# Optimization experiments

Hardware: AMD Instinct MI355X
Metric: run time of the kernel (lower is better)

The kernel has to match this reference:

```python
import jax, jax.numpy as jnp
import numpy as np

B, S, D_MODEL, N_HEADS, D_FEAT = 8, 1024, 1024, 16, 64


def setup_inputs() -> dict:
    key = jax.random.key(0)
    ks = jax.random.split(key, 5)
    sin = jax.random.normal(ks[0], (B, S, D_MODEL), dtype=jnp.float32)
    mask = jnp.ones((B, S), dtype=bool)  # only its presence matters in the original
    # Per-head Linear(d_model -> d_feature): weight stored as [H, d_model, d_feature]
    lim = 1.0 / np.sqrt(D_MODEL)
    Wx = jax.random.uniform(ks[1], (N_HEADS, D_MODEL, D_FEAT), dtype=jnp.float32, minval=-lim, maxval=lim)
    bx = jax.random.uniform(ks[2], (N_HEADS, D_FEAT), dtype=jnp.float32, minval=-lim, maxval=lim)
    # Output projection Linear(H*d_feature -> d_model), stored as [in, out]
    lim_p = 1.0 / np.sqrt(N_HEADS * D_FEAT)
    Wp = jax.random.uniform(ks[3], (N_HEADS * D_FEAT, D_MODEL), dtype=jnp.float32, minval=-lim_p, maxval=lim_p)
    bp = jax.random.uniform(ks[4], (D_MODEL,), dtype=jnp.float32, minval=-lim_p, maxval=lim_p)
    return {"sin": sin, "mask": mask, "Wx": Wx, "bx": bx, "Wp": Wp, "bp": bp}


def reference(sin, mask, Wx, bx, Wp, bp):
    # All heads batched: per-head linear projection  [B,H,S,F]
    x = jnp.einsum("bsd,hdf->bhsf", sin, Wx) + bx[None, :, None, :]
    # Cosine-similarity scores: x x^T / (||x|| ||x||^T)  -> [B,H,S,S]
    norm = jnp.sqrt(jnp.sum(x * x, axis=-1, keepdims=True))  # [B,H,S,1]
    scores = jnp.einsum("bhsf,bhtf->bhst", x, x) / (norm * jnp.swapaxes(norm, -2, -1))
    # Original quirk: when mask is not None, entries that are exactly 0.0 get -inf
    scores = jnp.where(scores == 0.0, -jnp.inf, scores)
    p_attn = jax.nn.softmax(scores, axis=-1)
    out = jnp.einsum("bhst,bhtf->bhsf", p_attn, x)
    # Concat heads: [B,S,H*F]
    out = jnp.transpose(out, (0, 2, 1, 3)).reshape(out.shape[0], out.shape[2], -1)
    return out @ Wp + bp
```

## Files before the change

### kernel.cpp

```cpp
#include <hip/hip_runtime.h>
#include <hip/hip_bf16.h>
#include <math.h>

typedef _Float16 f16;
typedef _Float16 half8 __attribute__((ext_vector_type(8)));
typedef float f32x4 __attribute__((ext_vector_type(4)));
typedef float f32x16 __attribute__((ext_vector_type(16)));
typedef unsigned int u32;

#define NB 8
#define NS 1024
#define DM 1024
#define NH 16
#define NF 64

__global__ __launch_bounds__(256) void csin_kernel(const float* __restrict__ in, f16* __restrict__ out) {
  long gid = (long)blockIdx.x * 256 + threadIdx.x;
  const float4* p = (const float4*)(in + gid * 8);
  float4 a = p[0], b = p[1];
  half8 v;
  v[0] = (f16)a.x; v[1] = (f16)a.y; v[2] = (f16)a.z; v[3] = (f16)a.w;
  v[4] = (f16)b.x; v[5] = (f16)b.y; v[6] = (f16)b.z; v[7] = (f16)b.w;
  *(half8*)(out + gid * 8) = v;
}

__global__ __launch_bounds__(256) void cwx_kernel(const float* __restrict__ Wx, f16* __restrict__ W2T) {
  __shared__ float T[64][65];
  int h = blockIdx.x >> 4, d0 = (blockIdx.x & 15) * 64;
  int tid = threadIdx.x;
  const float* src = Wx + ((size_t)h * 1024 + d0) * 64;
  int row = tid >> 2, cg = (tid & 3) * 16;
#pragma unroll
  for (int k = 0; k < 4; ++k) {
    float4 v = *(const float4*)(src + (size_t)row * 64 + cg + k * 4);
    T[row][cg + k * 4 + 0] = v.x;
    T[row][cg + k * 4 + 1] = v.y;
    T[row][cg + k * 4 + 2] = v.z;
    T[row][cg + k * 4 + 3] = v.w;
  }
  __syncthreads();
  int f = tid >> 2, dg = (tid & 3) * 16;
  f16 o[16];
#pragma unroll
  for (int j = 0; j < 16; ++j) o[j] = (f16)T[dg + j][f];
  *(half8*)(W2T + (size_t)(h * 64 + f) * DM + d0 + dg) = *(half8*)&o[0];
  *(half8*)(W2T + (size_t)(h * 64 + f) * DM + d0 + dg + 8) = *(half8*)&o[8];
}

__global__ __launch_bounds__(256) void cwp_kernel(const float* __restrict__ Wp, f16* __restrict__ WpT) {
  __shared__ float T[64][65];
  int n0 = (blockIdx.x >> 4) * 64, d0 = (blockIdx.x & 15) * 64;
  int tid = threadIdx.x;
  int row = tid >> 2, cg = (tid & 3) * 16;
#pragma unroll
  for (int k = 0; k < 4; ++k) {
    float4 v = *(const float4*)(Wp + (size_t)(d0 + row) * DM + n0 + cg + k * 4);
    T[row][cg + k * 4 + 0] = v.x;
    T[row][cg + k * 4 + 1] = v.y;
    T[row][cg + k * 4 + 2] = v.z;
    T[row][cg + k * 4 + 3] = v.w;
  }
  __syncthreads();
  int f = tid >> 2, dg = (tid & 3) * 16;
  f16 o[16];
#pragma unroll
  for (int j = 0; j < 16; ++j) o[j] = (f16)T[dg + j][f];
  *(half8*)(WpT + (size_t)(n0 + f) * DM + d0 + dg) = *(half8*)&o[0];
  *(half8*)(WpT + (size_t)(n0 + f) * DM + d0 + dg + 8) = *(half8*)&o[8];
}

template <int MODE>
__global__ __launch_bounds__(256) void gemm_kernel(const f16* __restrict__ A, const f16* __restrict__ Bt,
                                                   const float* __restrict__ bias, void* __restrict__ Cv) {
  __shared__ f16 As[128][64];
  __shared__ f16 Bs[128][64];
  int tid = threadIdx.x;
  int l = tid & 63, wv = tid >> 6;
  int wm = wv >> 1, wn = wv & 1;
  int xcd = blockIdx.x & 7, m = blockIdx.x >> 3;
  int bm = ((m >> 3) << 3) | xcd;
  int bn = m & 7;
  int lr = l & 15, lh = l >> 4;

  f32x4 acc[4][4];
#pragma unroll
  for (int i = 0; i < 4; ++i)
#pragma unroll
    for (int j = 0; j < 4; ++j) acc[i][j] = (f32x4)0.f;

  const f16* gA = A + (size_t)(bm * 128 + wv * 32 + (l >> 3)) * DM + (l & 7) * 8;
  const f16* gB = Bt + (size_t)(bn * 128 + wv * 32 + (l >> 3)) * DM + (l & 7) * 8;
  f16* ldsA = &As[wv * 32][0];
  f16* ldsB = &Bs[wv * 32][0];

  for (int k0 = 0; k0 < DM; k0 += 64) {
    __syncthreads();
#pragma unroll
    for (int c = 0; c < 4; ++c) {
      __builtin_amdgcn_global_load_lds(
          (const __attribute__((address_space(1))) void*)(gA + k0 + (size_t)c * 8 * DM),
          (__attribute__((address_space(3))) void*)(ldsA + c * 512), 16, 0, 0);
      __builtin_amdgcn_global_load_lds(
          (const __attribute__((address_space(1))) void*)(gB + k0 + (size_t)c * 8 * DM),
          (__attribute__((address_space(3))) void*)(ldsB + c * 512), 16, 0, 0);
    }
    __syncthreads();
#pragma unroll
    for (int ks = 0; ks < 2; ++ks) {
      half8 af[4], bf[4];
#pragma unroll
      for (int mi = 0; mi < 4; ++mi) af[mi] = *(const half8*)&As[wm * 64 + mi * 16 + lr][ks * 32 + lh * 8];
#pragma unroll
      for (int ni = 0; ni < 4; ++ni) bf[ni] = *(const half8*)&Bs[wn * 64 + ni * 16 + lr][ks * 32 + lh * 8];
#pragma unroll
      for (int mi = 0; mi < 4; ++mi)
#pragma unroll
        for (int ni = 0; ni < 4; ++ni)
          acc[mi][ni] = __builtin_amdgcn_mfma_f32_16x16x32_f16(af[mi], bf[ni], acc[mi][ni], 0, 0, 0);
    }
  }

#pragma unroll
  for (int mi = 0; mi < 4; ++mi)
#pragma unroll
    for (int ni = 0; ni < 4; ++ni) {
      int gc = bn * 128 + wn * 64 + ni * 16 + lr;
      float bv = bias[gc];
#pragma unroll
      for (int r = 0; r < 4; ++r) {
        int gr = bm * 128 + wm * 64 + mi * 16 + lh * 4 + r;
        float v = acc[mi][ni][r] + bv;
        if (MODE == 0) {
          f16* x = (f16*)Cv;
          int b = gr >> 10, s = gr & 1023, h = gc >> 6, f = gc & 63;
          x[(size_t)((b * NH + h) * NS + s) * NF + f] = (f16)v;
        } else {
          ((float*)Cv)[(size_t)gr * DM + gc] = v;
        }
      }
    }
}

__global__ __launch_bounds__(256) void transnorm_kernel(f16* __restrict__ x, f16* __restrict__ xT) {
  __shared__ f16 T[64][64];
  __shared__ float sinv[64];
  int bh = blockIdx.x >> 4, s0 = (blockIdx.x & 15) * 64;
  int tid = threadIdx.x;
  f16* xb = x + (size_t)bh * (NS * NF);
  half8 vv[2];
#pragma unroll
  for (int it = 0; it < 2; ++it) {
    int idx = it * 256 + tid;
    int sr = idx >> 3, fcb = idx & 7;
    half8 v = *(const half8*)(xb + (size_t)(s0 + sr) * NF + fcb * 8);
    vv[it] = v;
    *(half8*)&T[sr][((fcb ^ ((sr >> 3) & 7)) * 8)] = v;
    float s = 0.f;
#pragma unroll
    for (int j = 0; j < 8; ++j) {
      float u = (float)v[j];
      s += u * u;
    }
    s += __shfl_xor(s, 1, 64);
    s += __shfl_xor(s, 2, 64);
    s += __shfl_xor(s, 4, 64);
    if ((tid & 7) == 0) sinv[sr] = rsqrtf(s);
  }
  __syncthreads();
#pragma unroll
  for (int it = 0; it < 2; ++it) {
    int idx = it * 256 + tid;
    int fr = idx >> 3, scb = idx & 7;
    half8 v;
#pragma unroll
    for (int j = 0; j < 8; ++j) v[j] = T[scb * 8 + j][(((fr >> 3) ^ scb) * 8) + (fr & 7)];
    *(half8*)(xT + ((size_t)bh * NF + fr) * NS + s0 + scb * 8) = v;
  }
#pragma unroll
  for (int it = 0; it < 2; ++it) {
    int idx = it * 256 + tid;
    int sr = idx >> 3, fcb = idx & 7;
    float inv = sinv[sr];
    half8 v = vv[it], o;
#pragma unroll
    for (int j = 0; j < 8; ++j) o[j] = (f16)((float)v[j] * inv);
    *(half8*)(xb + (size_t)(s0 + sr) * NF + fcb * 8) = o;
  }
}

__global__ __launch_bounds__(256, 4) void attn_kernel(const f16* __restrict__ xn, const f16* __restrict__ xT,
                                                      f16* __restrict__ ao) {
  __shared__ f16 KB[2][4096];
  __shared__ f16 VB[2][4096];

  int tid = threadIdx.x;
  int l = tid & 63, wv = tid >> 6;
  int lq = l & 31, hi = l >> 5;
  int kq = hi * 8;
  int xcd = blockIdx.x & 7, m = blockIdx.x >> 3;
  int bh = ((m >> 3) << 3) | xcd;
  int q0 = (m & 7) * 128;
  const f16* xnb = xn + (size_t)bh * (NS * NF);
  const f16* xTb = xT + (size_t)bh * (NF * NS);

  int srow = wv * 8 + (l >> 3);
  int scol = ((l & 7) ^ (l >> 3)) * 8;
  const f16* gK0 = xnb + (size_t)srow * NF + scol;
  const f16* gV0 = xTb + (size_t)srow * NS + scol;

  half8 bq[4];
#pragma unroll
  for (int ks = 0; ks < 4; ++ks)
    bq[ks] = *(const half8*)(xnb + (size_t)(q0 + wv * 32 + lq) * NF + ks * 16 + kq);

  f32x16 accO[2];
  accO[0] = (f32x16)0.f;
  accO[1] = (f32x16)0.f;
  float rs = 0.f;

#define STAGE(buf, t0_)                                                                               \
  do {                                                                                                \
    __builtin_amdgcn_global_load_lds(                                                                 \
        (const __attribute__((address_space(1))) void*)(gK0 + (size_t)(t0_) * NF),                    \
        (__attribute__((address_space(3))) void*)(&KB[buf][wv * 512]), 16, 0, 0);                     \
    __builtin_amdgcn_global_load_lds(                                                                 \
        (const __attribute__((address_space(1))) void*)(gK0 + (size_t)(t0_ + 32) * NF),               \
        (__attribute__((address_space(3))) void*)(&KB[buf][2048 + wv * 512]), 16, 0, 0);              \
    __builtin_amdgcn_global_load_lds(                                                                 \
        (const __attribute__((address_space(1))) void*)(gV0 + (t0_)),                                 \
        (__attribute__((address_space(3))) void*)(&VB[buf][wv * 512]), 16, 0, 0);                     \
    __builtin_amdgcn_global_load_lds(                                                                 \
        (const __attribute__((address_space(1))) void*)(gV0 + (size_t)32 * NS + (t0_)),               \
        (__attribute__((address_space(3))) void*)(&VB[buf][2048 + wv * 512]), 16, 0, 0);              \
  } while (0)

  const float L2E = 1.4426950408889634f;

  STAGE(0, 0);
  asm volatile("s_waitcnt vmcnt(0)" ::: "memory");
  __syncthreads();

  int cur = 0;
  for (int t = 0; t < 16; ++t) {
    if (t < 15) STAGE(cur ^ 1, (t + 1) * 64);

    const char* kb = (const char*)&KB[cur][0];
    const char* vb = (const char*)&VB[cur][0];

#pragma unroll
    for (int ti = 0; ti < 2; ++ti) {
      half8 ak[4];
#pragma unroll
      for (int ks = 0; ks < 4; ++ks)
        ak[ks] = *(const half8*)(kb + (ti * 32 + lq) * 128 + ((((ks * 2 + hi)) ^ (lq & 7)) << 4));

      f32x16 sa = (f32x16)0.f;
      __builtin_amdgcn_s_setprio(1);
#pragma unroll
      for (int ks = 0; ks < 4; ++ks)
        sa = __builtin_amdgcn_mfma_f32_32x32x16_f16(ak[ks], bq[ks], sa, 0, 0, 0);
      __builtin_amdgcn_s_setprio(0);

      u32 pk[8];
#pragma unroll
      for (int mm = 0; mm < 8; ++mm) {
        float a = sa[2 * mm], b = sa[2 * mm + 1];
        float ea = (a == 0.f) ? 0.f : exp2f(__builtin_fmaf(a, L2E, -L2E));
        float eb = (b == 0.f) ? 0.f : exp2f(__builtin_fmaf(b, L2E, -L2E));
        rs += ea + eb;
        auto h = __builtin_amdgcn_cvt_pkrtz(ea, eb);
        pk[mm] = __builtin_bit_cast(u32, h);
      }
      uint4 a0, a1;
#if __has_builtin(__builtin_amdgcn_permlane32_swap)
      {
        auto s02 = __builtin_amdgcn_permlane32_swap((int)pk[0], (int)pk[2], false, false);
        auto s13 = __builtin_amdgcn_permlane32_swap((int)pk[1], (int)pk[3], false, false);
        auto s46 = __builtin_amdgcn_permlane32_swap((int)pk[4], (int)pk[6], false, false);
        auto s57 = __builtin_amdgcn_permlane32_swap((int)pk[5], (int)pk[7], false, false);
        a0.x = (u32)s02[0]; a0.z = (u32)s02[1];
        a0.y = (u32)s13[0]; a0.w = (u32)s13[1];
        a1.x = (u32)s46[0]; a1.z = (u32)s46[1];
        a1.y = (u32)s57[0]; a1.w = (u32)s57[1];
      }
#else
      {
        u32 sw[8];
#pragma unroll
        for (int mm = 0; mm < 8; ++mm) sw[mm] = (u32)__shfl_xor((int)pk[mm], 32, 64);
        bool lo = (hi == 0);
        a0.x = lo ? pk[0] : sw[2];
        a0.y = lo ? pk[1] : sw[3];
        a0.z = lo ? sw[0] : pk[2];
        a0.w = lo ? sw[1] : pk[3];
        a1.x = lo ? pk[4] : sw[6];
        a1.y = lo ? pk[5] : sw[7];
        a1.z = lo ? sw[4] : pk[6];
        a1.w = lo ? sw[5] : pk[7];
      }
#endif
      half8 pa0 = __builtin_bit_cast(half8, a0);
      half8 pa1 = __builtin_bit_cast(half8, a1);
      __builtin_amdgcn_s_setprio(1);
#pragma unroll
      for (int sub = 0; sub < 2; ++sub) {
        half8 pa = sub ? pa1 : pa0;
#pragma unroll
        for (int ni = 0; ni < 2; ++ni) {
          half8 vbf = *(const half8*)(vb + (ni * 32 + lq) * 128 + (((ti * 4 + sub * 2 + hi) ^ (lq & 7)) << 4));
          accO[ni] = __builtin_amdgcn_mfma_f32_32x32x16_f16(pa, vbf, accO[ni], 0, 0, 0);
        }
      }
      __builtin_amdgcn_s_setprio(0);
    }

    asm volatile("s_waitcnt vmcnt(0)" ::: "memory");
    __syncthreads();
    cur ^= 1;
  }
#undef STAGE

  rs += __shfl_xor(rs, 32, 64);

  int b = bh >> 4, h = bh & 15;
#pragma unroll
  for (int r = 0; r < 16; ++r) {
    int qoff = (r & 3) + 8 * (r >> 2) + 4 * hi;
    float rv = __shfl(rs, qoff, 64);
    float rinv = 1.0f / rv;
    int qg = q0 + wv * 32 + qoff;
#pragma unroll
    for (int ni = 0; ni < 2; ++ni) {
      int f = ni * 32 + lq;
      ao[((size_t)(b * NS + qg)) * DM + h * NF + f] = (f16)(accO[ni][r] * rinv);
    }
  }
}

extern "C" void kernel_launch(void* const* d_in, const int* in_sizes, int n_in,
                              void* d_out, int out_size, void* d_ws, size_t ws_size,
                              hipStream_t stream) {
  const float* sin_in = (const float*)d_in[0];
  const float* Wx = (const float*)d_in[2];
  const float* bx = (const float*)d_in[3];
  const float* Wp = (const float*)d_in[4];
  const float* bp = (const float*)d_in[5];
  float* out = (float*)d_out;

  char* p = (char*)d_ws;
  f16* sinb = (f16*)p;                      p += (size_t)NB * NS * DM * 2;
  f16* x    = (f16*)p;                      p += (size_t)NB * NH * NS * NF * 2;
  f16* xT   = (f16*)p;                      p += (size_t)NB * NH * NF * NS * 2;
  f16* W2T  = (f16*)p;                      p += (size_t)DM * DM * 2;
  f16* WpT  = (f16*)p;                      p += (size_t)DM * DM * 2;
  f16* ao   = sinb;

  csin_kernel<<<4096, 256, 0, stream>>>(sin_in, sinb);
  cwx_kernel<<<256, 256, 0, stream>>>(Wx, W2T);
  cwp_kernel<<<256, 256, 0, stream>>>(Wp, WpT);
  gemm_kernel<0><<<512, 256, 0, stream>>>(sinb, W2T, bx, (void*)x);
  transnorm_kernel<<<2048, 256, 0, stream>>>(x, xT);
  attn_kernel<<<1024, 256, 0, stream>>>(x, xT, ao);
  gemm_kernel<1><<<512, 256, 0, stream>>>(ao, WpT, bp, (void*)out);
}
```

Baseline: 223.6 us.

## Fuse fp32-to-fp16 input cast into projection GEMM and compute row sums via MFMA

The separate cast kernel for the input activations is removed. The first GEMM now reads fp32 rows directly, converts them to fp16 in registers and writes them to LDS, which saves a full round trip of the activation tensor through global memory and one launch. In the attention kernel, the softmax row-sum is no longer accumulated with scalar adds and cross-lane shuffles. Instead it is computed with two extra MFMAs of the packed probabilities against a ones vector, which also rounds the summed terms to fp16, matching the terms used in the PV product. The trade-off is that the GEMM's A-operand load is now synchronous through registers instead of the async global-to-LDS path, which may reduce overlap.

```diff
diff --git a/kernel.cpp b/kernel.cpp
--- a/kernel.cpp
+++ b/kernel.cpp
@@ -13,16 +13,6 @@
 #define DM 1024
 #define NH 16
 #define NF 64
-
-__global__ __launch_bounds__(256) void csin_kernel(const float* __restrict__ in, f16* __restrict__ out) {
-  long gid = (long)blockIdx.x * 256 + threadIdx.x;
-  const float4* p = (const float4*)(in + gid * 8);
-  float4 a = p[0], b = p[1];
-  half8 v;
-  v[0] = (f16)a.x; v[1] = (f16)a.y; v[2] = (f16)a.z; v[3] = (f16)a.w;
-  v[4] = (f16)b.x; v[5] = (f16)b.y; v[6] = (f16)b.z; v[7] = (f16)b.w;
-  *(half8*)(out + gid * 8) = v;
-}
 
 __global__ __launch_bounds__(256) void cwx_kernel(const float* __restrict__ Wx, f16* __restrict__ W2T) {
   __shared__ float T[64][65];
@@ -70,7 +60,7 @@
 }
 
 template <int MODE>
-__global__ __launch_bounds__(256) void gemm_kernel(const f16* __restrict__ A, const f16* __restrict__ Bt,
+__global__ __launch_bounds__(256) void gemm_kernel(const void* __restrict__ Av, const f16* __restrict__ Bt,
                                                    const float* __restrict__ bias, void* __restrict__ Cv) {
   __shared__ f16 As[128][64];
   __shared__ f16 Bs[128][64];
@@ -88,8 +78,10 @@
 #pragma unroll
     for (int j = 0; j < 4; ++j) acc[i][j] = (f32x4)0.f;
 
-  const f16* gA = A + (size_t)(bm * 128 + wv * 32 + (l >> 3)) * DM + (l & 7) * 8;
-  const f16* gB = Bt + (size_t)(bn * 128 + wv * 32 + (l >> 3)) * DM + (l & 7) * 8;
+  int arow = bm * 128 + wv * 32 + (l >> 3), acol = (l & 7) * 8;
+  const f16* gA = (const f16*)Av + (size_t)arow * DM + acol;
+  const float* gAf = (const float*)Av + (size_t)arow * DM + acol;
+  const f16* gB = Bt + (size_t)(bn * 128 + wv * 32 + (l >> 3)) * DM + acol;
   f16* ldsA = &As[wv * 32][0];
   f16* ldsB = &Bs[wv * 32][0];
 
@@ -97,9 +89,20 @@
     __syncthreads();
 #pragma unroll
     for (int c = 0; c < 4; ++c) {
-      __builtin_amdgcn_global_load_lds(
-          (const __attribute__((address_space(1))) void*)(gA + k0 + (size_t)c * 8 * DM),
-          (__attribute__((address_space(3))) void*)(ldsA + c * 512), 16, 0, 0);
+      if (MODE == 0) {
+        const float* s = gAf + k0 + (size_t)c * 8 * DM;
+        float4 u = *(const float4*)s, w = *(const float4*)(s + 4);
+        uint4 hw;
+        hw.x = __builtin_bit_cast(u32, __builtin_amdgcn_cvt_pkrtz(u.x, u.y));
+        hw.y = __builtin_bit_cast(u32, __builtin_amdgcn_cvt_pkrtz(u.z, u.w));
+        hw.z = __builtin_bit_cast(u32, __builtin_amdgcn_cvt_pkrtz(w.x, w.y));
+        hw.w = __builtin_bit_cast(u32, __builtin_amdgcn_cvt_pkrtz(w.z, w.w));
+        *(half8*)(ldsA + c * 512 + l * 8) = __builtin_bit_cast(half8, hw);
+      } else {
+        __builtin_amdgcn_global_load_lds(
+            (const __attribute__((address_space(1))) void*)(gA + k0 + (size_t)c * 8 * DM),
+            (__attribute__((address_space(3))) void*)(ldsA + c * 512), 16, 0, 0);
+      }
       __builtin_amdgcn_global_load_lds(
           (const __attribute__((address_space(1))) void*)(gB + k0 + (size_t)c * 8 * DM),
           (__attribute__((address_space(3))) void*)(ldsB + c * 512), 16, 0, 0);
@@ -213,10 +216,14 @@
   for (int ks = 0; ks < 4; ++ks)
     bq[ks] = *(const half8*)(xnb + (size_t)(q0 + wv * 32 + lq) * NF + ks * 16 + kq);
 
-  f32x16 accO[2];
+  half8 ones;
+#pragma unroll
+  for (int j = 0; j < 8; ++j) ones[j] = (f16)1.0f;
+
+  f32x16 accO[2], accR;
   accO[0] = (f32x16)0.f;
   accO[1] = (f32x16)0.f;
-  float rs = 0.f;
+  accR = (f32x16)0.f;
 
 #define STAGE(buf, t0_)                                                                               \
   do {                                                                                                \
@@ -267,7 +274,6 @@
         float a = sa[2 * mm], b = sa[2 * mm + 1];
         float ea = (a == 0.f) ? 0.f : exp2f(__builtin_fmaf(a, L2E, -L2E));
         float eb = (b == 0.f) ? 0.f : exp2f(__builtin_fmaf(b, L2E, -L2E));
-        rs += ea + eb;
         auto h = __builtin_amdgcn_cvt_pkrtz(ea, eb);
         pk[mm] = __builtin_bit_cast(u32, h);
       }
@@ -302,6 +308,8 @@
       half8 pa0 = __builtin_bit_cast(half8, a0);
       half8 pa1 = __builtin_bit_cast(half8, a1);
       __builtin_amdgcn_s_setprio(1);
+      accR = __builtin_amdgcn_mfma_f32_32x32x16_f16(pa0, ones, accR, 0, 0, 0);
+      accR = __builtin_amdgcn_mfma_f32_32x32x16_f16(pa1, ones, accR, 0, 0, 0);
 #pragma unroll
       for (int sub = 0; sub < 2; ++sub) {
         half8 pa = sub ? pa1 : pa0;
@@ -320,14 +328,11 @@
   }
 #undef STAGE
 
-  rs += __shfl_xor(rs, 32, 64);
-
   int b = bh >> 4, h = bh & 15;
 #pragma unroll
   for (int r = 0; r < 16; ++r) {
     int qoff = (r & 3) + 8 * (r >> 2) + 4 * hi;
-    float rv = __shfl(rs, qoff, 64);
-    float rinv = 1.0f / rv;
+    float rinv = 1.0f / accR[r];
     int qg = q0 + wv * 32 + qoff;
 #pragma unroll
     for (int ni = 0; ni < 2; ++ni) {
@@ -348,18 +353,16 @@
   float* out = (float*)d_out;
 
   char* p = (char*)d_ws;
-  f16* sinb = (f16*)p;                      p += (size_t)NB * NS * DM * 2;
+  f16* ao   = (f16*)p;                      p += (size_t)NB * NS * DM * 2;
   f16* x    = (f16*)p;                      p += (size_t)NB * NH * NS * NF * 2;
   f16* xT   = (f16*)p;                      p += (size_t)NB * NH * NF * NS * 2;
   f16* W2T  = (f16*)p;                      p += (size_t)DM * DM * 2;
   f16* WpT  = (f16*)p;                      p += (size_t)DM * DM * 2;
-  f16* ao   = sinb;
-
-  csin_kernel<<<4096, 256, 0, stream>>>(sin_in, sinb);
+
   cwx_kernel<<<256, 256, 0, stream>>>(Wx, W2T);
   cwp_kernel<<<256, 256, 0, stream>>>(Wp, WpT);
-  gemm_kernel<0><<<512, 256, 0, stream>>>(sinb, W2T, bx, (void*)x);
+  gemm_kernel<0><<<512, 256, 0, stream>>>((const void*)sin_in, W2T, bx, (void*)x);
   transnorm_kernel<<<2048, 256, 0, stream>>>(x, xT);
   attn_kernel<<<1024, 256, 0, stream>>>(x, xT, ao);
-  gemm_kernel<1><<<512, 256, 0, stream>>>(ao, WpT, bp, (void*)out);
-}
+  gemm_kernel<1><<<512, 256, 0, stream>>>((const void*)ao, WpT, bp, (void*)out);
+}
```

Measured after the change: 222.5 us. Within noise of the previous version (-0.5%).
